# Performance work log

Hardware: AMD Instinct MI355X
Metric: run time of the kernel (lower is better)

## Reference

```python
import jax, jax.numpy as jnp
import numpy as np

B, CIN, HID, T, W, H, TAU = 8, 16, 64, 4, 32, 32, 5
EPS = 1e-5
DN = ('NCDHW', 'OIDHW', 'NCDHW')


def conv3d(x, w, b):
    # 'same' conv3d, NCDHW layout
    y = jax.lax.conv_general_dilated(x, w, (1, 1, 1), 'SAME', dimension_numbers=DN)
    return y + b[None, :, None, None, None]


def ln3(u):
    # F.layer_norm over the last 3 (spatial) dims, no affine
    mu = jnp.mean(u, axis=(-3, -2, -1), keepdims=True)
    var = jnp.var(u, axis=(-3, -2, -1), keepdims=True)
    return (u - mu) * jax.lax.rsqrt(var + EPS)


def ln4(u, w, b):
    # nn.LayerNorm(memory_shape): over last 4 dims (C,T,W,H), with affine
    mu = jnp.mean(u, axis=(-4, -3, -2, -1), keepdims=True)
    var = jnp.var(u, axis=(-4, -3, -2, -1), keepdims=True)
    return (u - mu) * jax.lax.rsqrt(var + EPS) * w + b


def self_attention(r, c_history):
    scale = 1.0 / np.sqrt(T * W * H)
    scores = jnp.einsum('bctwh,lbctwh->bl', r, c_history) * scale  # [B, TAU]
    # faithful to source: softmax over dim=0 (the batch axis of the [b,l] scores)
    attn = jax.nn.softmax(scores, axis=0)
    return jnp.einsum('bl,lbctwh->bctwh', attn, c_history)


def setup_inputs() -> dict:
    key = jax.random.key(0)
    ks = jax.random.split(key, 8)
    x = jax.random.normal(ks[0], (B, CIN, T, W, H), jnp.float32)
    c_history = jax.random.normal(ks[1], (TAU, B, HID, T, W, H), jnp.float32)
    m = jax.random.normal(ks[2], (B, HID, T, W, H), jnp.float32)
    h = jax.random.normal(ks[3], (B, HID, T, W, H), jnp.float32)
    Wx = jax.random.normal(ks[4], (7, HID, CIN, 3, 3, 3), jnp.float32) * 0.05
    bx = jnp.zeros((7, HID), jnp.float32)
    # 9 state-branch conv kernels: [hr, hi, hg, mi', mg', mf', ho, co, mo]
    Wh = jax.random.normal(ks[5], (9, HID, HID, 3, 3, 3), jnp.float32) * 0.02
    bh = jnp.zeros((9, HID), jnp.float32)
    w111 = jax.random.normal(ks[6], (HID, 2 * HID, 1, 1, 1), jnp.float32) * 0.05
    b111 = jnp.zeros((HID,), jnp.float32)
    ln_w = jnp.ones((HID, T, W, H), jnp.float32)
    ln_b = jnp.zeros((HID, T, W, H), jnp.float32)
    return dict(x=x, c_history=c_history, m=m, h=h, Wx=Wx, bx=bx, Wh=Wh, bh=bh,
                w111=w111, b111=b111, ln_w=ln_w, ln_b=ln_b)


def reference(x, c_history, m, h, Wx, bx, Wh, bh, w111, b111, ln_w, ln_b):
    cx = lambda i: conv3d(x, Wx[i], bx[i])
    cs = lambda u, i: conv3d(u, Wh[i], bh[i])
    r = jax.nn.sigmoid(ln3(cx(0) + cs(h, 0)))
    i = jax.nn.sigmoid(ln3(cx(1) + cs(h, 1)))
    g = jnp.tanh(ln3(cx(2) + cs(h, 2)))
    recall = self_attention(r, c_history)
    c = i * g + ln4(c_history[-1] + recall, ln_w, ln_b)
    i_p = jax.nn.sigmoid(ln3(cx(3) + cs(m, 3)))
    g_p = jnp.tanh(ln3(cx(4) + cs(m, 4)))
    f_p = jax.nn.sigmoid(ln3(cx(5) + cs(m, 5)))
    m_new = i_p * g_p + f_p * m
    o = jax.nn.sigmoid(ln3(cx(6) + cs(h, 6) + cs(c, 7) + cs(m_new, 8)))
    h_new = o * jnp.tanh(conv3d(jnp.concatenate([c, m_new], axis=1), w111, b111))
    c_history_new = jnp.concatenate([c_history[1:], c[None]], axis=0)
    return (c_history_new, m_new, h_new)
```

## Files before the change

kernel.cpp:

```cpp
#include <hip/hip_runtime.h>
#include <hip/hip_bf16.h>
#include <math.h>

#define BATCH 8
#define CIN 16
#define HID 64
#define S2 1024
#define SP 4096
#define CHB 262144
#define TAU 5
#define GATE_SZ 2097152
#define EPS 1e-5f

#define WS_Z_OFF   ((size_t)3 * GATE_SZ)
#define WS_ST_OFF  ((size_t)4 * GATE_SZ)

typedef unsigned short u16;
typedef __attribute__((ext_vector_type(8))) short  short8;
typedef __attribute__((ext_vector_type(8))) u16    ushort8;
typedef __attribute__((ext_vector_type(4))) float  f32x4;

#define N7 (7*27*64*96)
#define NO (27*64*128)
#define N1 (64*128)

__device__ __forceinline__ u16 f2b(float v) {
    __hip_bfloat16 h = __float2bfloat16(v);
    u16 r; __builtin_memcpy(&r, &h, 2); return r;
}

__device__ __forceinline__ float* gate_ptr(float* out, float* ws, int g) {
    return (g < 4) ? (out + (size_t)g * GATE_SZ) : (ws + (size_t)(g - 4) * GATE_SZ);
}

__device__ __forceinline__ float fsig(float v) {
    v = fminf(fmaxf(v, -30.f), 30.f);
    return 1.f / (1.f + __expf(-v));
}
__device__ __forceinline__ float ftanh(float v) {
    v = fminf(fmaxf(v, -15.f), 15.f);
    const float t = __expf(-2.f * v);
    return (1.f - t) / (1.f + t);
}

__global__ __launch_bounds__(256) void pack_w_k(const float* __restrict__ Wx,
                                                const float* __restrict__ Wh,
                                                const float* __restrict__ w111,
                                                u16* __restrict__ A7, u16* __restrict__ Ao,
                                                u16* __restrict__ A111,
                                                float* __restrict__ stats,
                                                float* __restrict__ sums)
{
    const int idx = blockIdx.x * 256 + threadIdx.x;
    if (idx < 128)  stats[idx] = 0.f;
    if (idx < 7168) sums[idx] = 0.f;
    if (idx < N7) {
        const int k = idx % 96, oc = (idx / 96) % 64, tap = (idx / (96*64)) % 27, g = idx / (96*64*27);
        float v = 0.f;
        if (k < 16)      v = Wx[((size_t)(g*64 + oc)*16 + k)      * 27 + tap];
        else if (k < 80) v = Wh[((size_t)(g*64 + oc)*64 + (k-16)) * 27 + tap];
        A7[idx] = f2b(v);
    } else if (idx < N7 + NO) {
        const int j = idx - N7;
        const int k = j % 128, oc = (j / 128) % 64, tap = j / (128*64);
        float v = (k < 64) ? Wh[((size_t)(7*64 + oc)*64 + k)      * 27 + tap]
                           : Wh[((size_t)(8*64 + oc)*64 + (k-64)) * 27 + tap];
        Ao[j] = f2b(v);
    } else if (idx < N7 + NO + N1) {
        const int j = idx - N7 - NO;
        A111[j] = f2b(w111[j]);
    }
}

__global__ __launch_bounds__(256) void pack_xhm_k(const float* __restrict__ x,
                                                  const float* __restrict__ h,
                                                  const float* __restrict__ m,
                                                  u16* __restrict__ XH, u16* __restrict__ XM)
{
    __shared__ float t[144][65];
    const int bi = blockIdx.x, b = bi >> 6, s0 = (bi & 63) << 6;
    for (int i = threadIdx.x; i < 144*64; i += 256) {
        const int row = i >> 6, sc = i & 63;
        float v;
        if (row < 16)      v = x[((size_t)b*16 + row)      * SP + s0 + sc];
        else if (row < 80) v = h[((size_t)b*64 + (row-16)) * SP + s0 + sc];
        else               v = m[((size_t)b*64 + (row-80)) * SP + s0 + sc];
        t[row][sc] = v;
    }
    __syncthreads();
    for (int j = threadIdx.x; j < 64*96; j += 256) {
        const int s = j / 96, ch = j % 96;
        const size_t o = ((size_t)b*4096 + s0 + s) * 96 + ch;
        XH[o] = f2b(ch < 80 ? t[ch][s] : 0.f);
        XM[o] = f2b(ch < 16 ? t[ch][s] : (ch < 80 ? t[ch + 64][s] : 0.f));
    }
}

template<int KCH, int TAPS, int NR, int MODE, int MT, int MINW>
__global__ __launch_bounds__(256, MINW) void conv_mfma_k(
    const u16* __restrict__ XA, const u16* __restrict__ XB,
    const u16* __restrict__ Apack,
    const float* __restrict__ bxp, const float* __restrict__ bhp,
    const float* __restrict__ b111,
    float* __restrict__ out, float* __restrict__ ws,
    float* __restrict__ sums)
{
    constexpr int YT   = NR + 2;
    constexpr int ROWS = 4 * YT * 34;
    constexpr int PADK = 40;
    __shared__ __align__(16) u16 xs[ROWS * PADK];

    const int bi = blockIdx.x;
    int g = 0, b, y0, ocb = 0;
    const u16* X; const u16* Ag; float* outp;
    if (MODE == 0) {
        constexpr int YB = 32 / NR;
        g  = bi / (8 * YB);
        b  = (bi / YB) % 8;
        y0 = (bi % YB) * NR;
        X  = (g >= 3 && g <= 5) ? XB : XA;
        Ag = Apack + (size_t)g * TAPS * 64 * KCH;
        outp = gate_ptr(out, ws, g) + (size_t)b * CHB;
    } else if (MODE == 1) {
        ocb = (bi & 1) * 32;
        b  = bi >> 6;
        y0 = (bi >> 1) & 31;
        X = XA; Ag = Apack;
        outp = ws + (size_t)2 * GATE_SZ + (size_t)b * CHB;
    } else {
        b = bi >> 5; y0 = bi & 31;
        X = XA; Ag = Apack;
        outp = ws + (size_t)b * CHB;
    }
    const u16* Xb = X + (size_t)b * 4096 * KCH;

    const int tid  = threadIdx.x;
    const int w    = tid >> 6;
    const int lane = tid & 63;
    const int xn   = lane & 15, quad = lane >> 4;

    f32x4 acc[MT][2 * NR] = {};

    for (int kc = 0; kc < KCH / 32; ++kc) {
        if (kc != 0) __syncthreads();
        for (int cix = tid; cix < ROWS * 4; cix += 256) {
            const int r = cix >> 2, sub = cix & 3;
            const int t = r / (YT * 34), rem = r % (YT * 34);
            const int yy = rem / 34, xx = rem % 34;
            const int gy = y0 + yy - 1, gx = xx - 1;
            ushort8 v = {0, 0, 0, 0, 0, 0, 0, 0};
            if ((unsigned)gy < 32u && (unsigned)gx < 32u)
                v = *(const ushort8*)&Xb[(size_t)(t * 1024 + gy * 32 + gx) * KCH + kc * 32 + sub * 8];
            *(ushort8*)&xs[r * PADK + sub * 8] = v;
        }
        __syncthreads();

        auto load_a = [&](short8* a, int tap) {
            #pragma unroll
            for (int mt = 0; mt < MT; ++mt)
                a[mt] = *(const short8*)
                    &Ag[(size_t)(tap * 64 + ocb + mt * 16 + xn) * KCH + kc * 32 + quad * 8];
        };
        auto load_b = [&](short8* bf, int tap) {
            int kd, ky, kx;
            if (TAPS == 27) { kd = tap / 9; ky = (tap / 3) % 3; kx = tap % 3; }
            else            { kd = 1; ky = 1; kx = 1; }
            const int tin = w + kd - 1;
            #pragma unroll
            for (int nt = 0; nt < 2 * NR; ++nt) {
                const int ysub = nt >> 1, xh = nt & 1;
                bf[nt] = *(const short8*)
                    &xs[((tin * YT + ysub + ky) * 34 + xh * 16 + xn + kx) * PADK + quad * 8];
            }
        };
        auto do_mfma = [&](short8* a, short8* bf) {
            #pragma unroll
            for (int nt = 0; nt < 2 * NR; ++nt)
                #pragma unroll
                for (int mt = 0; mt < MT; ++mt)
                    acc[mt][nt] = __builtin_amdgcn_mfma_f32_16x16x32_bf16(a[mt], bf[nt], acc[mt][nt], 0, 0, 0);
        };

        if (TAPS == 27) {
            const int tap_lo = (w == 0) ? 9 : 0;
            const int tap_hi = (w == 3) ? 18 : 27;
            short8 a0[MT], b0[2 * NR], a1[MT], b1[2 * NR];
            load_a(a0, tap_lo); load_b(b0, tap_lo);
            int tap = tap_lo;
            for (; tap + 2 <= tap_hi; tap += 2) {
                load_a(a1, tap + 1); load_b(b1, tap + 1);
                do_mfma(a0, b0);
                if (tap + 2 < tap_hi) { load_a(a0, tap + 2); load_b(b0, tap + 2); }
                do_mfma(a1, b1);
            }
            if (tap < tap_hi) do_mfma(a0, b0);
        } else {
            short8 a0[MT], b0[2 * NR];
            load_a(a0, 0); load_b(b0, 0);
            do_mfma(a0, b0);
        }
    }

    constexpr bool SUMS1 = (MODE == 1);
    #pragma unroll
    for (int mt = 0; mt < MT; ++mt)
    #pragma unroll
    for (int reg = 0; reg < 4; ++reg) {
        const int oc = ocb + mt * 16 + quad * 4 + reg;
        float bias;
        if (MODE == 0)      bias = bxp[g * 64 + oc] + bhp[g * 64 + oc];
        else if (MODE == 1) bias = bhp[7 * 64 + oc] + bhp[8 * 64 + oc];
        else                bias = b111[oc];
        float s = 0.f, s2 = 0.f;
        #pragma unroll
        for (int nt = 0; nt < 2 * NR; ++nt) {
            const int ysub = nt >> 1, xh = nt & 1;
            const int sp = w * 1024 + (y0 + ysub) * 32 + xh * 16 + xn;
            float* p = outp + (size_t)oc * SP + sp;
            float vv = acc[mt][nt][reg] + bias;
            if (MODE == 1) vv += *p;
            *p = vv;
            s += vv; s2 += vv * vv;
        }
        if ((MODE == 0 && g < 6) || SUMS1) {
            #pragma unroll
            for (int off = 8; off > 0; off >>= 1) {
                s  += __shfl_xor(s, off);
                s2 += __shfl_xor(s2, off);
            }
            if (xn == 0) {
                const int gs = SUMS1 ? 6 : g;
                float* dst = &sums[(size_t)((gs * 8 + b) * 64 + oc) * 2];
                atomicAdd(dst, s);
                atomicAdd(dst + 1, s2);
            }
        }
    }
}

__global__ __launch_bounds__(256) void scores_k(const float* __restrict__ u0,
                                                const float* __restrict__ chist,
                                                const float* __restrict__ sums,
                                                float* __restrict__ stats)
{
    const int blk = blockIdx.x;
    const int b = blk >> 6, chn = blk & 63;
    const float* sp2 = &sums[(size_t)(b * 64 + chn) * 2];
    const float mu = sp2[0] * (1.f / SP);
    const float var = sp2[1] * (1.f / SP) - mu * mu;
    const float rr = rsqrtf(var + EPS);
    const float* rp = u0 + (size_t)b * CHB;
    const int lo = chn * SP;
    float s[TAU] = {};
    for (int k = lo + threadIdx.x; k < lo + SP; k += 256) {
        const float rv = fsig((rp[k] - mu) * rr);
        #pragma unroll
        for (int l = 0; l < TAU; ++l) s[l] += rv * chist[(size_t)(l * BATCH + b) * CHB + k];
    }
    __shared__ float rsh[TAU][4];
    #pragma unroll
    for (int l = 0; l < TAU; ++l) {
        float v = s[l];
        #pragma unroll
        for (int off = 32; off > 0; off >>= 1) v += __shfl_down(v, off);
        if ((threadIdx.x & 63) == 0) rsh[l][threadIdx.x >> 6] = v;
    }
    __syncthreads();
    if (threadIdx.x < TAU) {
        const int l = threadIdx.x;
        atomicAdd(&stats[l * 8 + b],
                  (rsh[l][0] + rsh[l][1] + rsh[l][2] + rsh[l][3]) * (1.f / 64.f));
    }
}

__global__ __launch_bounds__(256) void recall_k(const float* __restrict__ chist,
                                                float* __restrict__ ws,
                                                float* __restrict__ part)
{
    const float* stats = ws + WS_ST_OFF;
    const int blk = blockIdx.x;
    const int b = blk >> 10;
    const int idx = (blk & 1023) * 256 + threadIdx.x;

    __shared__ float attn[TAU];
    if (threadIdx.x < TAU) {
        const int l = threadIdx.x;
        float mx = -1e30f;
        for (int bb = 0; bb < BATCH; ++bb) mx = fmaxf(mx, stats[l * 8 + bb]);
        float sum = 0.f, e = 0.f;
        for (int bb = 0; bb < BATCH; ++bb) {
            float t = __expf(stats[l * 8 + bb] - mx);
            sum += t;
            if (bb == b) e = t;
        }
        attn[l] = e / sum;
    }
    __syncthreads();
    const float a0 = attn[0], a1 = attn[1], a2 = attn[2], a3 = attn[3], a4 = attn[4];

    const size_t e = (size_t)b * CHB + idx;
    const size_t LB = (size_t)BATCH * CHB;
    float z = chist[4 * LB + e] * (1.f + a4)
            + a0 * chist[0 * LB + e] + a1 * chist[1 * LB + e]
            + a2 * chist[2 * LB + e] + a3 * chist[3 * LB + e];
    ws[WS_Z_OFF + e] = z;

    float s = z, s2 = z * z;
    #pragma unroll
    for (int off = 32; off > 0; off >>= 1) { s += __shfl_down(s, off); s2 += __shfl_down(s2, off); }
    __shared__ float rs[4], rs2[4];
    if ((threadIdx.x & 63) == 0) { rs[threadIdx.x >> 6] = s; rs2[threadIdx.x >> 6] = s2; }
    __syncthreads();
    if (threadIdx.x == 0) {
        part[blk]        = rs[0] + rs[1] + rs[2] + rs[3];
        part[8192 + blk] = rs2[0] + rs2[1] + rs2[2] + rs2[3];
    }
}

__global__ __launch_bounds__(256) void cm_pcm_k(float* __restrict__ out, float* __restrict__ ws,
                                                const float* __restrict__ m,
                                                const float* __restrict__ lnw,
                                                const float* __restrict__ lnb,
                                                const float* __restrict__ part,
                                                const float* __restrict__ sums,
                                                u16* __restrict__ PCM)
{
    __shared__ __align__(16) u16 tl[64][136];
    __shared__ float lst[5][64][2];
    const int bi = blockIdx.x;
    const int b = bi >> 6;
    const int s0 = (bi & 63) << 6;

    for (int j = threadIdx.x; j < 5 * 64; j += 256) {
        const int gg = j >> 6, chn = j & 63;
        const float* sp2 = &sums[(size_t)(((gg + 1) * 8 + b) * 64 + chn) * 2];
        const float mu_ = sp2[0] * (1.f / SP);
        const float var_ = sp2[1] * (1.f / SP) - mu_ * mu_;
        lst[gg][chn][0] = mu_;
        lst[gg][chn][1] = rsqrtf(var_ + EPS);
    }
    float s = 0.f, s2 = 0.f;
    for (int j = threadIdx.x; j < 1024; j += 256) {
        s  += part[b * 1024 + j];
        s2 += part[8192 + b * 1024 + j];
    }
    #pragma unroll
    for (int off = 32; off > 0; off >>= 1) { s += __shfl_down(s, off); s2 += __shfl_down(s2, off); }
    __shared__ float rs[4], rs2[4], st[2];
    if ((threadIdx.x & 63) == 0) { rs[threadIdx.x >> 6] = s; rs2[threadIdx.x >> 6] = s2; }
    __syncthreads();
    if (threadIdx.x == 0) {
        float S  = rs[0] + rs[1] + rs[2] + rs[3];
        float Sq = rs2[0] + rs2[1] + rs2[2] + rs2[3];
        float mu  = S * (1.f / CHB);
        float var = Sq * (1.f / CHB) - mu * mu;
        st[0] = mu; st[1] = rsqrtf(var + EPS);
    }
    __syncthreads();
    const float mu = st[0], rstd = st[1];

    for (int i = threadIdx.x; i < 1024; i += 256) {
        const int chn = i >> 4;
        const int sp4 = (i & 15) << 2;
        const size_t e = (size_t)b * CHB + (size_t)chn * SP + s0 + sp4;
        const size_t le = (size_t)chn * SP + s0 + sp4;
        float4 z  = *(const float4*)&ws[WS_Z_OFF + e];
        float4 u1 = *(const float4*)&gate_ptr(out, ws, 1)[e];
        float4 u2 = *(const float4*)&gate_ptr(out, ws, 2)[e];
        float4 u3 = *(const float4*)&gate_ptr(out, ws, 3)[e];
        float4 u4 = *(const float4*)&gate_ptr(out, ws, 4)[e];
        float4 u5 = *(const float4*)&gate_ptr(out, ws, 5)[e];
        float4 mm = *(const float4*)&m[e];
        float4 lw = *(const float4*)&lnw[le];
        float4 lb = *(const float4*)&lnb[le];
        const float m1 = lst[0][chn][0], r1 = lst[0][chn][1];
        const float m2 = lst[1][chn][0], r2 = lst[1][chn][1];
        const float m3 = lst[2][chn][0], r3 = lst[2][chn][1];
        const float m4 = lst[3][chn][0], r4 = lst[3][chn][1];
        const float m5 = lst[4][chn][0], r5 = lst[4][chn][1];
        float4 c, mn;
        {
            const float uu1[4] = {u1.x, u1.y, u1.z, u1.w};
            const float uu2[4] = {u2.x, u2.y, u2.z, u2.w};
            const float uu3[4] = {u3.x, u3.y, u3.z, u3.w};
            const float uu4[4] = {u4.x, u4.y, u4.z, u4.w};
            const float uu5[4] = {u5.x, u5.y, u5.z, u5.w};
            const float zz[4]  = {z.x, z.y, z.z, z.w};
            const float mmv[4] = {mm.x, mm.y, mm.z, mm.w};
            const float lwv[4] = {lw.x, lw.y, lw.z, lw.w};
            const float lbv[4] = {lb.x, lb.y, lb.z, lb.w};
            float cv[4], mv[4];
            #pragma unroll
            for (int k = 0; k < 4; ++k) {
                const float gi = fsig ((uu1[k] - m1) * r1);
                const float gg = ftanh((uu2[k] - m2) * r2);
                const float ip = fsig ((uu3[k] - m3) * r3);
                const float gp = ftanh((uu4[k] - m4) * r4);
                const float fp = fsig ((uu5[k] - m5) * r5);
                cv[k] = gi * gg + (zz[k] - mu) * rstd * lwv[k] + lbv[k];
                mv[k] = ip * gp + fp * mmv[k];
                tl[sp4 + k][chn]      = f2b(cv[k]);
                tl[sp4 + k][64 + chn] = f2b(mv[k]);
            }
            c.x = cv[0]; c.y = cv[1]; c.z = cv[2]; c.w = cv[3];
            mn.x = mv[0]; mn.y = mv[1]; mn.z = mv[2]; mn.w = mv[3];
        }
        *(float4*)&out[(size_t)4 * GATE_SZ + e] = c;
        *(float4*)&out[(size_t)5 * GATE_SZ + e] = mn;
    }
    __syncthreads();
    for (int j = threadIdx.x; j < 1024; j += 256) {
        const int sidx = j >> 4, c8 = (j & 15) << 3;
        ushort8 v = *(const ushort8*)&tl[sidx][c8];
        *(ushort8*)&PCM[((size_t)b * 4096 + s0 + sidx) * 128 + c8] = v;
    }
}

__global__ __launch_bounds__(256) void tail_k(const float* __restrict__ chist,
                                              const float* __restrict__ u6,
                                              const float* __restrict__ v,
                                              const float* __restrict__ sums,
                                              float* __restrict__ out)
{
    const int bi = blockIdx.x;
    if (bi < 8192) {
        const size_t i = (size_t)bi * 256 + threadIdx.x;
        ((float4*)out)[i] = ((const float4*)(chist + GATE_SZ))[i];
    } else {
        const int j = bi - 8192;
        const size_t e0 = (size_t)j * 1024;
        const int b   = (int)(e0 >> 18);
        const int chn = (int)((e0 >> 12) & 63);
        const float* sp2 = &sums[(size_t)((6 * 8 + b) * 64 + chn) * 2];
        const float mu = sp2[0] * (1.f / SP);
        const float var = sp2[1] * (1.f / SP) - mu * mu;
        const float rr = rsqrtf(var + EPS);
        const size_t i = (size_t)j * 256 + threadIdx.x;
        float4 uv = ((const float4*)u6)[i], vv = ((const float4*)v)[i];
        float4 r;
        r.x = fsig((uv.x - mu) * rr) * ftanh(vv.x);
        r.y = fsig((uv.y - mu) * rr) * ftanh(vv.y);
        r.z = fsig((uv.z - mu) * rr) * ftanh(vv.z);
        r.w = fsig((uv.w - mu) * rr) * ftanh(vv.w);
        ((float4*)(out + (size_t)6 * GATE_SZ))[i] = r;
    }
}

extern "C" void kernel_launch(void* const* d_in, const int* in_sizes, int n_in,
                              void* d_out, int out_size, void* d_ws, size_t ws_size,
                              hipStream_t stream)
{
    const float* x    = (const float*)d_in[0];
    const float* ch   = (const float*)d_in[1];
    const float* m    = (const float*)d_in[2];
    const float* h    = (const float*)d_in[3];
    const float* Wx   = (const float*)d_in[4];
    const float* bx   = (const float*)d_in[5];
    const float* Wh   = (const float*)d_in[6];
    const float* bh   = (const float*)d_in[7];
    const float* w111 = (const float*)d_in[8];
    const float* b111 = (const float*)d_in[9];
    const float* lnw  = (const float*)d_in[10];
    const float* lnb  = (const float*)d_in[11];
    float* out = (float*)d_out;
    float* ws  = (float*)d_ws;

    u16* XH   = (u16*)(out + (size_t)4 * GATE_SZ);
    u16* A7   = (u16*)(out + (size_t)5 * GATE_SZ);
    u16* XM   = (u16*)(out + (size_t)6 * GATE_SZ);
    u16* Ao   = XM + (size_t)BATCH * 4096 * 96;
    u16* A111 = Ao + (size_t)NO;
    u16* PCM  = (u16*)out;
    float* part = (float*)(A111 + N1);
    float* sums = part + 16384;
    float* stats = ws + WS_ST_OFF;

    pack_w_k<<<(N7 + NO + N1 + 255) / 256, 256, 0, stream>>>(Wx, Wh, w111, A7, Ao, A111, stats, sums);
    pack_xhm_k<<<512, 256, 0, stream>>>(x, h, m, XH, XM);

    conv_mfma_k<96, 27, 2, 0, 4, 3><<<896, 256, 0, stream>>>(XH, XM, A7, bx, bh, nullptr, out, ws, sums);

    scores_k<<<512, 256, 0, stream>>>(out, ch, sums, stats);
    recall_k<<<8192, 256, 0, stream>>>(ch, ws, part);
    cm_pcm_k<<<512, 256, 0, stream>>>(out, ws, m, lnw, lnb, part, sums, PCM);

    conv_mfma_k<128, 27, 1, 1, 2, 4><<<512, 256, 0, stream>>>(PCM, nullptr, Ao, nullptr, bh, nullptr, out, ws, sums);
    conv_mfma_k<128, 1, 1, 2, 4, 3><<<256, 256, 0, stream>>>(PCM, nullptr, A111, nullptr, nullptr, b111, out, ws, nullptr);

    tail_k<<<10240, 256, 0, stream>>>(ch, ws + (size_t)2 * GATE_SZ, ws, sums, out);
}
```

Before: 408.4 us.

## Replace atomic LN stat accumulation with block partials and separate reduce kernel

The conv epilogue now reduces per-channel sum and sum-of-squares across the four waves in shared memory. Each block writes its partials to a dedicated slot instead of issuing global atomicAdds, and a small lnred kernel turns the partials into mean and rsqrt-variance used by later kernels. scores_k and recall_k are vectorised to float4 loads, and recall_k runs a quarter as many blocks with matching partial indexing. This removes atomic contention and the zero-init of the sums, at the cost of two extra tiny launches and a block-level sync in the conv epilogue.

```diff
diff --git a/kernel.cpp b/kernel.cpp
--- a/kernel.cpp
+++ b/kernel.cpp
@@ -23,6 +23,7 @@
 #define N7 (7*27*64*96)
 #define NO (27*64*128)
 #define N1 (64*128)
+#define NP2 65536
 
 __device__ __forceinline__ u16 f2b(float v) {
     __hip_bfloat16 h = __float2bfloat16(v);
@@ -48,12 +49,10 @@
                                                 const float* __restrict__ w111,
                                                 u16* __restrict__ A7, u16* __restrict__ Ao,
                                                 u16* __restrict__ A111,
-                                                float* __restrict__ stats,
-                                                float* __restrict__ sums)
+                                                float* __restrict__ stats)
 {
     const int idx = blockIdx.x * 256 + threadIdx.x;
-    if (idx < 128)  stats[idx] = 0.f;
-    if (idx < 7168) sums[idx] = 0.f;
+    if (idx < 128) stats[idx] = 0.f;
     if (idx < N7) {
         const int k = idx % 96, oc = (idx / 96) % 64, tap = (idx / (96*64)) % 27, g = idx / (96*64*27);
         float v = 0.f;
@@ -103,12 +102,13 @@
     const float* __restrict__ bxp, const float* __restrict__ bhp,
     const float* __restrict__ b111,
     float* __restrict__ out, float* __restrict__ ws,
-    float* __restrict__ sums)
+    float* __restrict__ p2s, float* __restrict__ p2s2)
 {
     constexpr int YT   = NR + 2;
     constexpr int ROWS = 4 * YT * 34;
     constexpr int PADK = 40;
     __shared__ __align__(16) u16 xs[ROWS * PADK];
+    __shared__ float red[4][MT * 16][2];
 
     const int bi = blockIdx.x;
     int g = 0, b, y0, ocb = 0;
@@ -201,61 +201,103 @@
         }
     }
 
-    constexpr bool SUMS1 = (MODE == 1);
+    const bool do_stats = (MODE == 1) || (MODE == 0 && g < 6);
     #pragma unroll
-    for (int mt = 0; mt < MT; ++mt)
-    #pragma unroll
-    for (int reg = 0; reg < 4; ++reg) {
-        const int oc = ocb + mt * 16 + quad * 4 + reg;
-        float bias;
-        if (MODE == 0)      bias = bxp[g * 64 + oc] + bhp[g * 64 + oc];
-        else if (MODE == 1) bias = bhp[7 * 64 + oc] + bhp[8 * 64 + oc];
-        else                bias = b111[oc];
-        float s = 0.f, s2 = 0.f;
+    for (int mt = 0; mt < MT; ++mt) {
+        float sA[4] = {}, s2A[4] = {};
         #pragma unroll
         for (int nt = 0; nt < 2 * NR; ++nt) {
             const int ysub = nt >> 1, xh = nt & 1;
             const int sp = w * 1024 + (y0 + ysub) * 32 + xh * 16 + xn;
-            float* p = outp + (size_t)oc * SP + sp;
-            float vv = acc[mt][nt][reg] + bias;
-            if (MODE == 1) vv += *p;
-            *p = vv;
-            s += vv; s2 += vv * vv;
-        }
-        if ((MODE == 0 && g < 6) || SUMS1) {
             #pragma unroll
-            for (int off = 8; off > 0; off >>= 1) {
-                s  += __shfl_xor(s, off);
-                s2 += __shfl_xor(s2, off);
+            for (int reg = 0; reg < 4; ++reg) {
+                const int oc = ocb + mt * 16 + quad * 4 + reg;
+                float bias;
+                if (MODE == 0)      bias = bxp[g * 64 + oc] + bhp[g * 64 + oc];
+                else if (MODE == 1) bias = bhp[7 * 64 + oc] + bhp[8 * 64 + oc];
+                else                bias = b111[oc];
+                float* p = outp + (size_t)oc * SP + sp;
+                float vv = acc[mt][nt][reg] + bias;
+                if (MODE == 1) vv += *p;
+                *p = vv;
+                if (MODE <= 1) { sA[reg] += vv; s2A[reg] += vv * vv; }
             }
-            if (xn == 0) {
-                const int gs = SUMS1 ? 6 : g;
-                float* dst = &sums[(size_t)((gs * 8 + b) * 64 + oc) * 2];
-                atomicAdd(dst, s);
-                atomicAdd(dst + 1, s2);
+        }
+        if (MODE <= 1 && do_stats) {
+            #pragma unroll
+            for (int reg = 0; reg < 4; ++reg) {
+                float s = sA[reg], s2 = s2A[reg];
+                #pragma unroll
+                for (int off = 8; off > 0; off >>= 1) {
+                    s  += __shfl_xor(s, off);
+                    s2 += __shfl_xor(s2, off);
+                }
+                if (xn == 0) {
+                    red[w][mt * 16 + quad * 4 + reg][0] = s;
+                    red[w][mt * 16 + quad * 4 + reg][1] = s2;
+                }
             }
         }
     }
+    if (MODE <= 1 && do_stats) {
+        __syncthreads();
+        if (tid < MT * 16) {
+            const float s  = red[0][tid][0] + red[1][tid][0] + red[2][tid][0] + red[3][tid][0];
+            const float s2 = red[0][tid][1] + red[1][tid][1] + red[2][tid][1] + red[3][tid][1];
+            const int oc = ocb + tid;
+            const int idx = (MODE == 0) ? ((g * 512 + b * 64 + oc) * 16 + (y0 >> 1))
+                                        : (49152 + (b * 64 + oc) * 32 + y0);
+            p2s[idx]  = s;
+            p2s2[idx] = s2;
+        }
+    }
+}
+
+__global__ __launch_bounds__(256) void lnred_k(const float* __restrict__ p2s,
+                                               const float* __restrict__ p2s2,
+                                               float* __restrict__ lnstats,
+                                               int e0, int e1, int ebase)
+{
+    const int e = e0 + blockIdx.x * 256 + threadIdx.x;
+    if (e >= e1) return;
+    const int g = e >> 9, bc = e & 511;
+    float s = 0.f, s2 = 0.f;
+    if (g < 6) {
+        const int base = e * 16;
+        #pragma unroll
+        for (int i = 0; i < 16; ++i) { s += p2s[base + i]; s2 += p2s2[base + i]; }
+    } else {
+        const int base = 49152 + bc * 32;
+        #pragma unroll
+        for (int i = 0; i < 32; ++i) { s += p2s[base + i]; s2 += p2s2[base + i]; }
+    }
+    const float mu = s * (1.f / SP);
+    const float var = s2 * (1.f / SP) - mu * mu;
+    lnstats[2 * (e - ebase)]     = mu;
+    lnstats[2 * (e - ebase) + 1] = rsqrtf(var + EPS);
 }
 
 __global__ __launch_bounds__(256) void scores_k(const float* __restrict__ u0,
                                                 const float* __restrict__ chist,
-                                                const float* __restrict__ sums,
+                                                const float* __restrict__ lnstats,
                                                 float* __restrict__ stats)
 {
     const int blk = blockIdx.x;
     const int b = blk >> 6, chn = blk & 63;
-    const float* sp2 = &sums[(size_t)(b * 64 + chn) * 2];
-    const float mu = sp2[0] * (1.f / SP);
-    const float var = sp2[1] * (1.f / SP) - mu * mu;
-    const float rr = rsqrtf(var + EPS);
-    const float* rp = u0 + (size_t)b * CHB;
-    const int lo = chn * SP;
+    const float mu = lnstats[2 * (b * 64 + chn)];
+    const float rr = lnstats[2 * (b * 64 + chn) + 1];
+    const float4* rp4 = (const float4*)(u0 + (size_t)b * CHB);
+    const int lo4 = chn * (SP / 4);
     float s[TAU] = {};
-    for (int k = lo + threadIdx.x; k < lo + SP; k += 256) {
-        const float rv = fsig((rp[k] - mu) * rr);
+    for (int k = lo4 + threadIdx.x; k < lo4 + SP / 4; k += 256) {
+        const float4 rv = rp4[k];
+        const float r0 = fsig((rv.x - mu) * rr), r1 = fsig((rv.y - mu) * rr);
+        const float r2 = fsig((rv.z - mu) * rr), r3 = fsig((rv.w - mu) * rr);
         #pragma unroll
-        for (int l = 0; l < TAU; ++l) s[l] += rv * chist[(size_t)(l * BATCH + b) * CHB + k];
+        for (int l = 0; l < TAU; ++l) {
+            const float4 c4 = ((const float4*)(chist + (size_t)(l * BATCH + b) * CHB))[k];
+            s[l] += r0 * c4.x + r1 * c4.y + r2 * c4.z + r3 * c4.w;
+        }
     }
     __shared__ float rsh[TAU][4];
     #pragma unroll
@@ -279,8 +321,8 @@
 {
     const float* stats = ws + WS_ST_OFF;
     const int blk = blockIdx.x;
-    const int b = blk >> 10;
-    const int idx = (blk & 1023) * 256 + threadIdx.x;
+    const int b = blk >> 8;
+    const int i4 = (blk & 255) * 256 + threadIdx.x;
 
     __shared__ float attn[TAU];
     if (threadIdx.x < TAU) {
@@ -298,14 +340,21 @@
     __syncthreads();
     const float a0 = attn[0], a1 = attn[1], a2 = attn[2], a3 = attn[3], a4 = attn[4];
 
-    const size_t e = (size_t)b * CHB + idx;
-    const size_t LB = (size_t)BATCH * CHB;
-    float z = chist[4 * LB + e] * (1.f + a4)
-            + a0 * chist[0 * LB + e] + a1 * chist[1 * LB + e]
-            + a2 * chist[2 * LB + e] + a3 * chist[3 * LB + e];
-    ws[WS_Z_OFF + e] = z;
-
-    float s = z, s2 = z * z;
+    const size_t e4  = (size_t)b * (CHB / 4) + i4;
+    const size_t LB4 = (size_t)BATCH * (CHB / 4);
+    const float4* c4 = (const float4*)chist;
+    const float4 h4 = c4[4 * LB4 + e4];
+    const float4 v0 = c4[0 * LB4 + e4], v1 = c4[1 * LB4 + e4];
+    const float4 v2 = c4[2 * LB4 + e4], v3 = c4[3 * LB4 + e4];
+    float4 z;
+    z.x = h4.x * (1.f + a4) + a0 * v0.x + a1 * v1.x + a2 * v2.x + a3 * v3.x;
+    z.y = h4.y * (1.f + a4) + a0 * v0.y + a1 * v1.y + a2 * v2.y + a3 * v3.y;
+    z.z = h4.z * (1.f + a4) + a0 * v0.z + a1 * v1.z + a2 * v2.z + a3 * v3.z;
+    z.w = h4.w * (1.f + a4) + a0 * v0.w + a1 * v1.w + a2 * v2.w + a3 * v3.w;
+    ((float4*)(ws + WS_Z_OFF))[e4] = z;
+
+    float s = z.x + z.y + z.z + z.w;
+    float s2 = z.x * z.x + z.y * z.y + z.z * z.z + z.w * z.w;
     #pragma unroll
     for (int off = 32; off > 0; off >>= 1) { s += __shfl_down(s, off); s2 += __shfl_down(s2, off); }
     __shared__ float rs[4], rs2[4];
@@ -313,7 +362,7 @@
     __syncthreads();
     if (threadIdx.x == 0) {
         part[blk]        = rs[0] + rs[1] + rs[2] + rs[3];
-        part[8192 + blk] = rs2[0] + rs2[1] + rs2[2] + rs2[3];
+        part[2048 + blk] = rs2[0] + rs2[1] + rs2[2] + rs2[3];
     }
 }
 
@@ -322,7 +371,7 @@
                                                 const float* __restrict__ lnw,
                                                 const float* __restrict__ lnb,
                                                 const float* __restrict__ part,
-                                                const float* __restrict__ sums,
+                                                const float* __restrict__ lnstats,
                                                 u16* __restrict__ PCM)
 {
     __shared__ __align__(16) u16 tl[64][136];
@@ -333,17 +382,11 @@
 
     for (int j = threadIdx.x; j < 5 * 64; j += 256) {
         const int gg = j >> 6, chn = j & 63;
-        const float* sp2 = &sums[(size_t)(((gg + 1) * 8 + b) * 64 + chn) * 2];
-        const float mu_ = sp2[0] * (1.f / SP);
-        const float var_ = sp2[1] * (1.f / SP) - mu_ * mu_;
-        lst[gg][chn][0] = mu_;
-        lst[gg][chn][1] = rsqrtf(var_ + EPS);
-    }
-    float s = 0.f, s2 = 0.f;
-    for (int j = threadIdx.x; j < 1024; j += 256) {
-        s  += part[b * 1024 + j];
-        s2 += part[8192 + b * 1024 + j];
-    }
+        lst[gg][chn][0] = lnstats[2 * ((gg + 1) * 512 + b * 64 + chn)];
+        lst[gg][chn][1] = lnstats[2 * ((gg + 1) * 512 + b * 64 + chn) + 1];
+    }
+    float s  = part[b * 256 + threadIdx.x];
+    float s2 = part[2048 + b * 256 + threadIdx.x];
     #pragma unroll
     for (int off = 32; off > 0; off >>= 1) { s += __shfl_down(s, off); s2 += __shfl_down(s2, off); }
     __shared__ float rs[4], rs2[4], st[2];
@@ -419,7 +462,7 @@
 __global__ __launch_bounds__(256) void tail_k(const float* __restrict__ chist,
                                               const float* __restrict__ u6,
                                               const float* __restrict__ v,
-                                              const float* __restrict__ sums,
+                                              const float* __restrict__ ln6,
                                               float* __restrict__ out)
 {
     const int bi = blockIdx.x;
@@ -431,10 +474,8 @@
         const size_t e0 = (size_t)j * 1024;
         const int b   = (int)(e0 >> 18);
         const int chn = (int)((e0 >> 12) & 63);
-        const float* sp2 = &sums[(size_t)((6 * 8 + b) * 64 + chn) * 2];
-        const float mu = sp2[0] * (1.f / SP);
-        const float var = sp2[1] * (1.f / SP) - mu * mu;
-        const float rr = rsqrtf(var + EPS);
+        const float mu = ln6[2 * (b * 64 + chn)];
+        const float rr = ln6[2 * (b * 64 + chn) + 1];
         const size_t i = (size_t)j * 256 + threadIdx.x;
         float4 uv = ((const float4*)u6)[i], vv = ((const float4*)v)[i];
         float4 r;
@@ -471,21 +512,26 @@
     u16* Ao   = XM + (size_t)BATCH * 4096 * 96;
     u16* A111 = Ao + (size_t)NO;
     u16* PCM  = (u16*)out;
-    float* part = (float*)(A111 + N1);
-    float* sums = part + 16384;
-    float* stats = ws + WS_ST_OFF;
-
-    pack_w_k<<<(N7 + NO + N1 + 255) / 256, 256, 0, stream>>>(Wx, Wh, w111, A7, Ao, A111, stats, sums);
+    float* part     = (float*)(A111 + N1);
+    float* p2s      = part + 4096;
+    float* p2s2     = p2s + NP2;
+    float* lnstatsA = p2s2 + NP2;
+    float* ln6      = ws + WS_Z_OFF;
+    float* stats    = ws + WS_ST_OFF;
+
+    pack_w_k<<<(N7 + NO + N1 + 255) / 256, 256, 0, stream>>>(Wx, Wh, w111, A7, Ao, A111, stats);
     pack_xhm_k<<<512, 256, 0, stream>>>(x, h, m, XH, XM);
 
-    conv_mfma_k<96, 27, 2, 0, 4, 3><<<896, 256, 0, stream>>>(XH, XM, A7, bx, bh, nullptr, out, ws, sums);
-
-    scores_k<<<512, 256, 0, stream>>>(out, ch, sums, stats);
-    recall_k<<<8192, 256, 0, stream>>>(ch, ws, part);
-    cm_pcm_k<<<512, 256, 0, stream>>>(out, ws, m, lnw, lnb, part, sums, PCM);
-
-    conv_mfma_k<128, 27, 1, 1, 2, 4><<<512, 256, 0, stream>>>(PCM, nullptr, Ao, nullptr, bh, nullptr, out, ws, sums);
-    conv_mfma_k<128, 1, 1, 2, 4, 3><<<256, 256, 0, stream>>>(PCM, nullptr, A111, nullptr, nullptr, b111, out, ws, nullptr);
-
-    tail_k<<<10240, 256, 0, stream>>>(ch, ws + (size_t)2 * GATE_SZ, ws, sums, out);
-}
+    conv_mfma_k<96, 27, 2, 0, 4, 3><<<896, 256, 0, stream>>>(XH, XM, A7, bx, bh, nullptr, out, ws, p2s, p2s2);
+    lnred_k<<<12, 256, 0, stream>>>(p2s, p2s2, lnstatsA, 0, 3072, 0);
+
+    scores_k<<<512, 256, 0, stream>>>(out, ch, lnstatsA, stats);
+    recall_k<<<2048, 256, 0, stream>>>(ch, ws, part);
+    cm_pcm_k<<<512, 256, 0, stream>>>(out, ws, m, lnw, lnb, part, lnstatsA, PCM);
+
+    conv_mfma_k<128, 27, 1, 1, 2, 4><<<512, 256, 0, stream>>>(PCM, nullptr, Ao, nullptr, bh, nullptr, out, ws, p2s, p2s2);
+    lnred_k<<<2, 256, 0, stream>>>(p2s, p2s2, ln6, 3072, 3584, 3072);
+    conv_mfma_k<128, 1, 1, 2, 4, 3><<<256, 256, 0, stream>>>(PCM, nullptr, A111, nullptr, nullptr, b111, out, ws, nullptr, nullptr);
+
+    tail_k<<<10240, 256, 0, stream>>>(ch, ws + (size_t)2 * GATE_SZ, ws, ln6, out);
+}
```

Measured after the change: 365.4 us. 10.5% less time.
